# Performance work log

Measured on AMD Instinct MI355X. Metric: run time of the kernel, lower is better.

The kernel has to match this reference:

```python
import jax, jax.numpy as jnp
import numpy as np

N, E, B = 100000, 3200000, 512
D_IN, D_H, HID = 500, 64, 200
NUM_CLASSES = 80
EPS_BN = 1e-5


def _sage(x, src, dst, Wl, bl, Wr):
    # PyG SAGEConv (mean aggr): out = lin_l(mean_{j->i} x_j) + lin_r(x_i)
    n = x.shape[0]
    agg = jax.ops.segment_sum(x[src], dst, num_segments=n)          # [n, d_in]
    deg = jax.ops.segment_sum(jnp.ones((src.shape[0],), x.dtype), dst, num_segments=n)
    mean = agg / jnp.maximum(deg, 1.0)[:, None]
    return mean @ Wl + bl + x @ Wr


def _bn(c, g, b):
    # BatchNorm1d, training-mode batch statistics (biased var)
    mu = c.mean(0)
    var = c.var(0)
    return (c - mu) / jnp.sqrt(var + EPS_BN) * g + b


def setup_inputs() -> dict:
    key = jax.random.key(0)
    ks = jax.random.split(key, 16)
    p = lambda k, shape: jax.random.normal(k, shape, dtype=jnp.float32) * 0.05
    z = lambda d: jnp.zeros((d,), jnp.float32)
    o = lambda d: jnp.ones((d,), jnp.float32)
    return {
        "x": jax.random.uniform(ks[0], (N, D_IN), dtype=jnp.float32),
        "edge_index": jax.random.randint(ks[1], (2, E), 0, N),
        "batch": jnp.sort(jax.random.randint(ks[2], (N,), 0, B)),
        "y": jax.random.randint(ks[3], (B,), 0, NUM_CLASSES),
        "conv1_Wl": p(ks[4], (D_IN, D_H)), "conv1_bl": z(D_H), "conv1_Wr": p(ks[5], (D_IN, D_H)),
        "conv2_Wl": p(ks[6], (D_H, D_H)),  "conv2_bl": z(D_H), "conv2_Wr": p(ks[7], (D_H, D_H)),
        "conv3_Wl": p(ks[8], (D_H, D_H)),  "conv3_bl": z(D_H), "conv3_Wr": p(ks[9], (D_H, D_H)),
        "lin1_W": p(ks[10], (D_H, HID)), "lin1_b": z(HID),
        "bn1_g": o(HID), "bn1_beta": z(HID),
        "lin2_W": p(ks[11], (HID, HID // 2)), "lin2_b": z(HID // 2),
        "bn2_g": o(HID // 2), "bn2_beta": z(HID // 2),
        "lin3_W": p(ks[12], (HID // 2, HID // 2)), "lin3_b": z(HID // 2),
        "bn3_g": o(HID // 2), "bn3_beta": z(HID // 2),
        "lin4_W": p(ks[13], (HID // 2, NUM_CLASSES)), "lin4_b": z(NUM_CLASSES),
    }


def reference(x, edge_index, batch, y,
              conv1_Wl, conv1_bl, conv1_Wr,
              conv2_Wl, conv2_bl, conv2_Wr,
              conv3_Wl, conv3_bl, conv3_Wr,
              lin1_W, lin1_b, bn1_g, bn1_beta,
              lin2_W, lin2_b, bn2_g, bn2_beta,
              lin3_W, lin3_b, bn3_g, bn3_beta,
              lin4_W, lin4_b):
    src, dst = edge_index[0], edge_index[1]
    # F.normalize(x, p=1.0, dim=-1)
    xn = x / jnp.maximum(jnp.abs(x).sum(-1, keepdims=True), 1e-12)
    e = _sage(xn, src, dst, conv1_Wl, conv1_bl, conv1_Wr)
    e = _sage(e, src, dst, conv2_Wl, conv2_bl, conv2_Wr)
    e = _sage(e, src, dst, conv3_Wl, conv3_bl, conv3_Wr)
    # global_mean_pool over graph ids
    sums = jax.ops.segment_sum(e, batch, num_segments=B)             # [B, 64]
    cnts = jax.ops.segment_sum(jnp.ones((e.shape[0],), e.dtype), batch, num_segments=B)
    c = sums / jnp.maximum(cnts, 1.0)[:, None]
    # dropout (p=0.1) omitted for a deterministic reference
    c = c @ lin1_W + lin1_b
    b = jnp.tanh(_bn(c, bn1_g, bn1_beta))
    c = b @ lin2_W + lin2_b
    b = jnp.tanh(_bn(c, bn2_g, bn2_beta))
    c = b @ lin3_W + lin3_b
    b = jnp.tanh(_bn(c, bn3_g, bn3_beta))
    return b @ lin4_W + lin4_b                                       # [B, 80]
```

## Files before the change

### kernel.cpp

```cpp
#include <hip/hip_runtime.h>
#include <hip/hip_bf16.h>

#define NN 100000
#define NE 3200000
#define NB 512
#define DIN 500
#define DH 64
#define HIDN 200
#define NCLS 80

#define NBUK 256
#define NPB 391
#define EPB 16384
#define NBLK_E ((NE + EPB - 1) / EPB)

typedef __attribute__((ext_vector_type(8))) short bf16x8;
typedef __attribute__((ext_vector_type(4))) float f32x4;

__device__ __forceinline__ short f2bf(float f) {
    union { float f; unsigned u; } v; v.f = f;
    unsigned r = v.u + 0x7FFF + ((v.u >> 16) & 1);
    return (short)(r >> 16);
}
__device__ __forceinline__ float bf2f(short s) {
    union { unsigned u; float f; } v; v.u = ((unsigned)(unsigned short)s) << 16;
    return v.f;
}

__global__ void bukhist_kernel(const int* __restrict__ dst, int* __restrict__ block_hist) {
    __shared__ int h[NBUK];
    for (int i = threadIdx.x; i < NBUK; i += 256) h[i] = 0;
    __syncthreads();
    int base = blockIdx.x * EPB;
    int end = min(base + EPB, NE);
    for (int e = base + threadIdx.x; e < end; e += 256)
        atomicAdd(&h[dst[e] / NPB], 1);
    __syncthreads();
    for (int i = threadIdx.x; i < NBUK; i += 256)
        block_hist[blockIdx.x * NBUK + i] = h[i];
}

__global__ void bukoff_kernel(int* __restrict__ block_hist, int* __restrict__ buk_base) {
    __shared__ int tot[NBUK];
    __shared__ int sc[NBUK];
    int b = threadIdx.x;
    int s = 0;
    for (int i = 0; i < NBLK_E; ++i) s += block_hist[i * NBUK + b];
    tot[b] = s; sc[b] = s;
    __syncthreads();
    for (int o = 1; o < NBUK; o <<= 1) {
        int t = (b >= o) ? sc[b - o] : 0;
        __syncthreads();
        sc[b] += t;
        __syncthreads();
    }
    int excl = sc[b] - tot[b];
    buk_base[b] = excl;
    if (b == NBUK - 1) buk_base[NBUK] = excl + tot[b];
    int run = excl;
    for (int i = 0; i < NBLK_E; ++i) {
        int idx = i * NBUK + b;
        int v = block_hist[idx];
        block_hist[idx] = run;
        run += v;
    }
}

__global__ void bukscat_kernel(const int* __restrict__ src, const int* __restrict__ dst,
                               const int* __restrict__ block_hist, int* __restrict__ bpack) {
    __shared__ int cur[NBUK];
    for (int i = threadIdx.x; i < NBUK; i += 256)
        cur[i] = block_hist[blockIdx.x * NBUK + i];
    __syncthreads();
    int base = blockIdx.x * EPB;
    int end = min(base + EPB, NE);
    for (int e = base + threadIdx.x; e < end; e += 256) {
        int d = dst[e];
        int bk = d / NPB;
        int p = atomicAdd(&cur[bk], 1);
        bpack[p] = (src[e] << 9) | (d - bk * NPB);
    }
}

__global__ void bukfin_kernel(const int* __restrict__ buk_base, const int* __restrict__ bpack,
                              int* __restrict__ row_ptr, float* __restrict__ invdeg,
                              int* __restrict__ csr_src) {
    __shared__ int cnt[NPB];
    __shared__ int cbase[NPB];
    int bk = blockIdx.x;
    int n0 = bk * NPB;
    int nloc = min(n0 + NPB, NN) - n0;
    for (int i = threadIdx.x; i < nloc; i += 256) cnt[i] = 0;
    __syncthreads();
    int beg = buk_base[bk], end = buk_base[bk + 1];
    for (int p = beg + threadIdx.x; p < end; p += 256)
        atomicAdd(&cnt[bpack[p] & 511], 1);
    __syncthreads();
    if (threadIdx.x == 0) {
        int run = beg;
        for (int i = 0; i < nloc; ++i) { int v = cnt[i]; cbase[i] = run; run += v; }
    }
    __syncthreads();
    for (int i = threadIdx.x; i < nloc; i += 256) {
        row_ptr[n0 + i] = cbase[i];
        invdeg[n0 + i] = 1.0f / fmaxf((float)cnt[i], 1.0f);
        cnt[i] = cbase[i];
    }
    if (bk == NBUK - 1 && threadIdx.x == 0) row_ptr[NN] = end;
    __syncthreads();
    for (int p = beg + threadIdx.x; p < end; p += 256) {
        int v = bpack[p];
        int q = atomicAdd(&cnt[v & 511], 1);
        csr_src[q] = v >> 9;
    }
}

__global__ void wprep_kernel(const float* __restrict__ Wl, const float* __restrict__ Wr,
                             short* __restrict__ Wb, int K, int KP) {
    int id = blockIdx.x * blockDim.x + threadIdx.x;
    if (id >= 128 * KP) return;
    int col = id / KP, k = id - col * KP;
    float v = 0.f;
    if (k < K) v = (col < 64) ? Wl[(size_t)k * 64 + col] : Wr[(size_t)k * 64 + (col - 64)];
    Wb[(size_t)col * KP + k] = f2bf(v);
}

__launch_bounds__(256)
__global__ void gemm_mfma_pipe(const float* __restrict__ in, const short* __restrict__ Wb,
                               short* __restrict__ Hl, float* __restrict__ Hr) {
    __shared__ short A_lds[2][128][40];
    __shared__ short B_lds[2][128][40];
    __shared__ float s_red[128][2];
    const int tid = threadIdx.x;
    const int row0 = blockIdx.x * 128;
    const int w = tid >> 6, l = tid & 63;
    const int q = l >> 4, r16 = l & 15;
    const int sa_row = tid >> 1;
    const int sa_kc  = (tid & 1) * 16;
    const int ga_row = row0 + sa_row;
    const bool row_ok = ga_row < NN;
    const float* arow = in + (size_t)ga_row * DIN + sa_kc;
    const short* bsrc = Wb + (size_t)sa_row * 512 + sa_kc;

    f32x4 acc0[8], acc1[8];
#pragma unroll
    for (int c = 0; c < 8; ++c) { acc0[c] = (f32x4){0.f,0.f,0.f,0.f}; acc1[c] = (f32x4){0.f,0.f,0.f,0.f}; }
    float pabs = 0.f;
    float va0[16], va1[16];
    bf16x8 vb00, vb01, vb10, vb11;

#define ISSUE(T, S) do { \
    _Pragma("unroll") \
    for (int i = 0; i < 16; i += 4) { \
        int gk = (T) * 32 + sa_kc + i; \
        float4 f = (row_ok && gk < DIN) ? *(const float4*)(arow + (T) * 32 + i) \
                                        : make_float4(0.f, 0.f, 0.f, 0.f); \
        va##S[i] = f.x; va##S[i+1] = f.y; va##S[i+2] = f.z; va##S[i+3] = f.w; \
    } \
    vb##S##0 = *(const bf16x8*)(bsrc + (T) * 32); \
    vb##S##1 = *(const bf16x8*)(bsrc + (T) * 32 + 8); \
} while (0)

#define STAGE(BUF, S) do { \
    short sh[16]; \
    _Pragma("unroll") \
    for (int i = 0; i < 16; ++i) { pabs += fabsf(va##S[i]); sh[i] = f2bf(va##S[i]); } \
    *(bf16x8*)&A_lds[BUF][sa_row][sa_kc]     = *(bf16x8*)&sh[0]; \
    *(bf16x8*)&A_lds[BUF][sa_row][sa_kc + 8] = *(bf16x8*)&sh[8]; \
    *(bf16x8*)&B_lds[BUF][sa_row][sa_kc]     = vb##S##0; \
    *(bf16x8*)&B_lds[BUF][sa_row][sa_kc + 8] = vb##S##1; \
} while (0)

#define COMPUTE(BUF) do { \
    bf16x8 a0 = *(bf16x8*)&A_lds[BUF][w * 32 + r16][q * 8]; \
    bf16x8 a1 = *(bf16x8*)&A_lds[BUF][w * 32 + 16 + r16][q * 8]; \
    _Pragma("unroll") \
    for (int c = 0; c < 8; ++c) { \
        bf16x8 b = *(bf16x8*)&B_lds[BUF][c * 16 + r16][q * 8]; \
        acc0[c] = __builtin_amdgcn_mfma_f32_16x16x32_bf16(a0, b, acc0[c], 0, 0, 0); \
        acc1[c] = __builtin_amdgcn_mfma_f32_16x16x32_bf16(a1, b, acc1[c], 0, 0, 0); \
    } \
} while (0)

    ISSUE(0, 0); ISSUE(1, 1);
    STAGE(0, 0);
    __syncthreads();
    for (int tt = 0; tt < 8; ++tt) {
        int t0 = tt * 2;
        if (tt < 7) ISSUE(t0 + 2, 0);
        COMPUTE(0);
        STAGE(1, 1);
        __syncthreads();
        if (tt < 7) ISSUE(t0 + 3, 1);
        COMPUTE(1);
        if (tt < 7) { STAGE(0, 0); __syncthreads(); }
    }
#undef ISSUE
#undef STAGE
#undef COMPUTE

    __syncthreads();
    s_red[sa_row][tid & 1] = pabs;
    __syncthreads();
    if (tid < 128) {
        float ss = s_red[tid][0] + s_red[tid][1];
        s_red[tid][0] = 1.0f / fmaxf(ss, 1e-12f);
    }
    __syncthreads();

#define EPI(RF, ACC) do { \
    _Pragma("unroll") \
    for (int c = 0; c < 8; ++c) { \
        _Pragma("unroll") \
        for (int rr = 0; rr < 4; ++rr) { \
            int lrow = w * 32 + (RF) * 16 + q * 4 + rr; \
            int grow = row0 + lrow; \
            if (grow < NN) { \
                float o = ACC[c][rr] * s_red[lrow][0]; \
                if (c < 4) Hl[(size_t)grow * 64 + c * 16 + r16] = f2bf(o); \
                else       Hr[(size_t)grow * 64 + (c - 4) * 16 + r16] = o; \
            } \
        } \
    } \
} while (0)
    EPI(0, acc0);
    EPI(1, acc1);
#undef EPI
}

__launch_bounds__(256)
__global__ void gemm64_mfma(const short* __restrict__ ein, const short* __restrict__ Wb,
                            short* __restrict__ Hl, float* __restrict__ Hr) {
    const int tid = threadIdx.x;
    const int row0 = blockIdx.x * 64;
    const int w = tid >> 6, l = tid & 63;
    const int q = l >> 4, r16 = l & 15;
    const int arow = row0 + w * 16 + r16;
    const bool ok = arow < NN;
    const short* ap = ein + (size_t)(ok ? arow : 0) * 64 + q * 8;
    f32x4 acc[8];
#pragma unroll
    for (int c = 0; c < 8; ++c) acc[c] = (f32x4){0.f, 0.f, 0.f, 0.f};
    const bf16x8 z8 = (bf16x8){0, 0, 0, 0, 0, 0, 0, 0};
#pragma unroll
    for (int t = 0; t < 2; ++t) {
        bf16x8 a = ok ? *(const bf16x8*)(ap + t * 32) : z8;
#pragma unroll
        for (int c = 0; c < 8; ++c) {
            bf16x8 b = *(const bf16x8*)(Wb + (size_t)(c * 16 + r16) * 64 + t * 32 + q * 8);
            acc[c] = __builtin_amdgcn_mfma_f32_16x16x32_bf16(a, b, acc[c], 0, 0, 0);
        }
    }
#pragma unroll
    for (int c = 0; c < 8; ++c) {
#pragma unroll
        for (int rr = 0; rr < 4; ++rr) {
            int grow = row0 + w * 16 + q * 4 + rr;
            if (grow < NN) {
                if (c < 4) Hl[(size_t)grow * 64 + c * 16 + r16] = f2bf(acc[c][rr]);
                else       Hr[(size_t)grow * 64 + (c - 4) * 16 + r16] = acc[c][rr];
            }
        }
    }
}

template<bool LAST>
__launch_bounds__(256, 8)
__global__ void gather_kernel(const int* __restrict__ row_ptr, const int* __restrict__ csr_src,
                              const short* __restrict__ Hl, const float* __restrict__ Hr,
                              const float* __restrict__ invdeg, const float* __restrict__ bl,
                              short* __restrict__ ebf, float* __restrict__ ef32) {
    int node = blockIdx.x * 4 + (threadIdx.x >> 6);
    if (node >= NN) return;
    int lane = threadIdx.x & 63;
    int ng = lane >> 3;
    int fl = lane & 7;
    int beg = row_ptr[node], end = row_ptr[node + 1];
    float a0[8], a1[8];
#pragma unroll
    for (int j = 0; j < 8; ++j) { a0[j] = 0.f; a1[j] = 0.f; }
    int p = beg + ng;
    for (; p + 24 < end; p += 32) {
        int s0 = csr_src[p];
        int s1 = csr_src[p + 8];
        int s2 = csr_src[p + 16];
        int s3 = csr_src[p + 24];
        bf16x8 v0 = *(const bf16x8*)(Hl + (size_t)s0 * 64 + fl * 8);
        bf16x8 v1 = *(const bf16x8*)(Hl + (size_t)s1 * 64 + fl * 8);
        bf16x8 v2 = *(const bf16x8*)(Hl + (size_t)s2 * 64 + fl * 8);
        bf16x8 v3 = *(const bf16x8*)(Hl + (size_t)s3 * 64 + fl * 8);
#pragma unroll
        for (int j = 0; j < 8; ++j) {
            a0[j] += bf2f(v0[j]) + bf2f(v2[j]);
            a1[j] += bf2f(v1[j]) + bf2f(v3[j]);
        }
    }
    for (; p < end; p += 8) {
        int s0 = csr_src[p];
        bf16x8 v0 = *(const bf16x8*)(Hl + (size_t)s0 * 64 + fl * 8);
#pragma unroll
        for (int j = 0; j < 8; ++j) a0[j] += bf2f(v0[j]);
    }
#pragma unroll
    for (int j = 0; j < 8; ++j) a0[j] += a1[j];
#pragma unroll
    for (int m = 8; m < 64; m <<= 1)
#pragma unroll
        for (int j = 0; j < 8; ++j) a0[j] += __shfl_xor(a0[j], m, 64);
    if (ng == 0) {
        float idg = invdeg[node];
        const float4 h0 = *(const float4*)(Hr + (size_t)node * 64 + fl * 8);
        const float4 h1 = *(const float4*)(Hr + (size_t)node * 64 + fl * 8 + 4);
        float o[8];
        o[0] = a0[0] * idg + bl[fl * 8 + 0] + h0.x;
        o[1] = a0[1] * idg + bl[fl * 8 + 1] + h0.y;
        o[2] = a0[2] * idg + bl[fl * 8 + 2] + h0.z;
        o[3] = a0[3] * idg + bl[fl * 8 + 3] + h0.w;
        o[4] = a0[4] * idg + bl[fl * 8 + 4] + h1.x;
        o[5] = a0[5] * idg + bl[fl * 8 + 5] + h1.y;
        o[6] = a0[6] * idg + bl[fl * 8 + 6] + h1.z;
        o[7] = a0[7] * idg + bl[fl * 8 + 7] + h1.w;
        if (LAST) {
            *(float4*)(ef32 + (size_t)node * 64 + fl * 8)     = make_float4(o[0], o[1], o[2], o[3]);
            *(float4*)(ef32 + (size_t)node * 64 + fl * 8 + 4) = make_float4(o[4], o[5], o[6], o[7]);
        } else {
            short s[8];
#pragma unroll
            for (int j = 0; j < 8; ++j) s[j] = f2bf(o[j]);
            *(bf16x8*)(ebf + (size_t)node * 64 + fl * 8) = *(bf16x8*)s;
        }
    }
}

__global__ void gseg_kernel(const int* __restrict__ batch, int* __restrict__ gstart) {
    int i = blockIdx.x * blockDim.x + threadIdx.x;
    if (i >= NN) return;
    int bc = batch[i];
    int bp = (i == 0) ? -1 : batch[i - 1];
    for (int b = bp + 1; b <= bc; ++b) gstart[b] = i;
    if (i == NN - 1)
        for (int b = bc + 1; b <= NB; ++b) gstart[b] = NN;
}

__launch_bounds__(256)
__global__ void pool_seg(const float* __restrict__ e, const int* __restrict__ gstart,
                         float* __restrict__ c0) {
    __shared__ float part[4][64];
    int b = blockIdx.x;
    int w = threadIdx.x >> 6, lane = threadIdx.x & 63;
    int s = gstart[b], t = gstart[b + 1];
    float acc = 0.f;
    for (int i = s + w; i < t; i += 4) acc += e[(size_t)i * 64 + lane];
    part[w][lane] = acc;
    __syncthreads();
    if (w == 0) {
        float v = part[0][lane] + part[1][lane] + part[2][lane] + part[3][lane];
        c0[b * 64 + lane] = v / fmaxf((float)(t - s), 1.0f);
    }
}

__global__ void lin_kernel(const float* __restrict__ in, const float* __restrict__ W,
                           const float* __restrict__ bias, float* __restrict__ out,
                           int Kd, int Dout) {
    int id = blockIdx.x * blockDim.x + threadIdx.x;
    if (id >= NB * Dout) return;
    int row = id / Dout, col = id - row * Dout;
    const float* ir = in + (size_t)row * Kd;
    float acc = bias[col];
    for (int k = 0; k < Kd; ++k) acc += ir[k] * W[(size_t)k * Dout + col];
    out[id] = acc;
}

__global__ void bnstats_kernel(const float* __restrict__ c, const float* __restrict__ g,
                               const float* __restrict__ beta, float* __restrict__ sa,
                               float* __restrict__ sb, int Dout) {
    int col = blockIdx.x;
    int tid = threadIdx.x;
    float s = 0.f, sq = 0.f;
    for (int r = tid; r < NB; r += 256) {
        float v = c[(size_t)r * Dout + col];
        s += v; sq += v * v;
    }
    __shared__ float ls[256], lq[256];
    ls[tid] = s; lq[tid] = sq;
    __syncthreads();
    for (int o = 128; o > 0; o >>= 1) {
        if (tid < o) { ls[tid] += ls[tid + o]; lq[tid] += lq[tid + o]; }
        __syncthreads();
    }
    if (tid == 0) {
        float mu = ls[0] / NB;
        float var = lq[0] / NB - mu * mu;
        float a = g[col] * rsqrtf(var + 1e-5f);
        sa[col] = a;
        sb[col] = beta[col] - mu * a;
    }
}

__global__ void bnapply_kernel(const float* __restrict__ c, const float* __restrict__ sa,
                               const float* __restrict__ sb, float* __restrict__ bv, int Dout) {
    int id = blockIdx.x * blockDim.x + threadIdx.x;
    if (id >= NB * Dout) return;
    int col = id % Dout;
    bv[id] = tanhf(c[id] * sa[col] + sb[col]);
}

extern "C" void kernel_launch(void* const* d_in, const int* in_sizes, int n_in,
                              void* d_out, int out_size, void* d_ws, size_t ws_size,
                              hipStream_t stream) {
    const float* x    = (const float*)d_in[0];
    const int* ei     = (const int*)d_in[1];
    const int* src    = ei;
    const int* dst    = ei + NE;
    const int* batch  = (const int*)d_in[2];
    const float* c1Wl = (const float*)d_in[4];
    const float* c1bl = (const float*)d_in[5];
    const float* c1Wr = (const float*)d_in[6];
    const float* c2Wl = (const float*)d_in[7];
    const float* c2bl = (const float*)d_in[8];
    const float* c2Wr = (const float*)d_in[9];
    const float* c3Wl = (const float*)d_in[10];
    const float* c3bl = (const float*)d_in[11];
    const float* c3Wr = (const float*)d_in[12];
    const float* l1W  = (const float*)d_in[13]; const float* l1b = (const float*)d_in[14];
    const float* bn1g = (const float*)d_in[15]; const float* bn1b = (const float*)d_in[16];
    const float* l2W  = (const float*)d_in[17]; const float* l2b = (const float*)d_in[18];
    const float* bn2g = (const float*)d_in[19]; const float* bn2b = (const float*)d_in[20];
    const float* l3W  = (const float*)d_in[21]; const float* l3b = (const float*)d_in[22];
    const float* bn3g = (const float*)d_in[23]; const float* bn3b = (const float*)d_in[24];
    const float* l4W  = (const float*)d_in[25]; const float* l4b = (const float*)d_in[26];
    float* out = (float*)d_out;

    char* wsb = (char*)d_ws;
    short* Hl     = (short*)wsb; wsb += (size_t)NN * 64 * 2;
    float* Hr     = (float*)wsb; wsb += (size_t)NN * 64 * 4;
    short* e      = (short*)wsb; wsb += (size_t)NN * 64 * 2;
    float* e3     = (float*)wsb; wsb += (size_t)NN * 64 * 4;
    float* invdeg = (float*)wsb; wsb += (size_t)NN * 4;
    float* c      = (float*)wsb; wsb += (size_t)NB * HIDN * 4;
    float* bv     = (float*)wsb; wsb += (size_t)NB * HIDN * 4;
    float* sa     = (float*)wsb; wsb += HIDN * 4;
    float* sb     = (float*)wsb; wsb += HIDN * 4;
    short* Wb1    = (short*)wsb; wsb += 128 * 512 * 2;
    short* Wb2    = (short*)wsb; wsb += 128 * 64 * 2;
    short* Wb3    = (short*)wsb; wsb += 128 * 64 * 2;
    int* row_ptr  = (int*)wsb;   wsb += (size_t)(NN + 1) * 4;
    int* csr_src  = (int*)wsb;   wsb += (size_t)NE * 4;
    int* buk_base = (int*)wsb;   wsb += (NBUK + 1) * 4;
    int* gstart   = (int*)wsb;   wsb += (NB + 1) * 4;
    int* bpack      = (int*)Hl;
    int* block_hist = (int*)e;

    bukhist_kernel<<<NBLK_E, 256, 0, stream>>>(dst, block_hist);
    bukoff_kernel<<<1, NBUK, 0, stream>>>(block_hist, buk_base);
    bukscat_kernel<<<NBLK_E, 256, 0, stream>>>(src, dst, block_hist, bpack);
    bukfin_kernel<<<NBUK, 256, 0, stream>>>(buk_base, bpack, row_ptr, invdeg, csr_src);

    gseg_kernel<<<(NN + 255) / 256, 256, 0, stream>>>(batch, gstart);

    wprep_kernel<<<(128 * 512 + 255) / 256, 256, 0, stream>>>(c1Wl, c1Wr, Wb1, DIN, 512);
    wprep_kernel<<<(128 * 64 + 255) / 256, 256, 0, stream>>>(c2Wl, c2Wr, Wb2, DH, 64);
    wprep_kernel<<<(128 * 64 + 255) / 256, 256, 0, stream>>>(c3Wl, c3Wr, Wb3, DH, 64);

    const int GB128 = (NN + 127) / 128;
    const int GB64  = (NN + 63) / 64;
    const int GGB   = (NN + 3) / 4;

    gemm_mfma_pipe<<<GB128, 256, 0, stream>>>(x, Wb1, Hl, Hr);
    gather_kernel<false><<<GGB, 256, 0, stream>>>(row_ptr, csr_src, Hl, Hr, invdeg, c1bl, e, e3);
    gemm64_mfma<<<GB64, 256, 0, stream>>>(e, Wb2, Hl, Hr);
    gather_kernel<false><<<GGB, 256, 0, stream>>>(row_ptr, csr_src, Hl, Hr, invdeg, c2bl, e, e3);
    gemm64_mfma<<<GB64, 256, 0, stream>>>(e, Wb3, Hl, Hr);
    gather_kernel<true><<<GGB, 256, 0, stream>>>(row_ptr, csr_src, Hl, Hr, invdeg, c3bl, e, e3);

    pool_seg<<<NB, 256, 0, stream>>>(e3, gstart, bv);

    lin_kernel<<<(NB * 200 + 255) / 256, 256, 0, stream>>>(bv, l1W, l1b, c, 64, 200);
    bnstats_kernel<<<200, 256, 0, stream>>>(c, bn1g, bn1b, sa, sb, 200);
    bnapply_kernel<<<(NB * 200 + 255) / 256, 256, 0, stream>>>(c, sa, sb, bv, 200);

    lin_kernel<<<(NB * 100 + 255) / 256, 256, 0, stream>>>(bv, l2W, l2b, c, 200, 100);
    bnstats_kernel<<<100, 256, 0, stream>>>(c, bn2g, bn2b, sa, sb, 100);
    bnapply_kernel<<<(NB * 100 + 255) / 256, 256, 0, stream>>>(c, sa, sb, bv, 100);

    lin_kernel<<<(NB * 100 + 255) / 256, 256, 0, stream>>>(bv, l3W, l3b, c, 100, 100);
    bnstats_kernel<<<100, 256, 0, stream>>>(c, bn3g, bn3b, sa, sb, 100);
    bnapply_kernel<<<(NB * 100 + 255) / 256, 256, 0, stream>>>(c, sa, sb, bv, 100);

    lin_kernel<<<(NB * 80 + 255) / 256, 256, 0, stream>>>(bv, l4W, l4b, out, 100, 80);
}
```

Before: 608.4 us.

## Replace LDS double-buffered first-layer GEMM with direct register-fed MFMA

The first SAGE layer GEMM no longer stages x and the bf16 weights through double-buffered shared memory. Each lane now loads its MFMA A fragment straight from global memory and reads weight fragments directly from global, which L1/L2 should serve. The row L1-norm is reduced with wave shuffles instead of a shared-memory reduction. Blocks shrink to 64 rows, which removes all barriers and LDS use but adds repeated weight reads from cache and less coalesced x loads.

```diff
diff --git a/kernel.cpp b/kernel.cpp
--- a/kernel.cpp
+++ b/kernel.cpp
@@ -126,106 +126,65 @@
 }
 
 __launch_bounds__(256)
-__global__ void gemm_mfma_pipe(const float* __restrict__ in, const short* __restrict__ Wb,
-                               short* __restrict__ Hl, float* __restrict__ Hr) {
-    __shared__ short A_lds[2][128][40];
-    __shared__ short B_lds[2][128][40];
-    __shared__ float s_red[128][2];
+__global__ void gemm_direct(const float* __restrict__ in, const short* __restrict__ Wb,
+                            short* __restrict__ Hl, float* __restrict__ Hr) {
     const int tid = threadIdx.x;
-    const int row0 = blockIdx.x * 128;
     const int w = tid >> 6, l = tid & 63;
     const int q = l >> 4, r16 = l & 15;
-    const int sa_row = tid >> 1;
-    const int sa_kc  = (tid & 1) * 16;
-    const int ga_row = row0 + sa_row;
-    const bool row_ok = ga_row < NN;
-    const float* arow = in + (size_t)ga_row * DIN + sa_kc;
-    const short* bsrc = Wb + (size_t)sa_row * 512 + sa_kc;
-
-    f32x4 acc0[8], acc1[8];
-#pragma unroll
-    for (int c = 0; c < 8; ++c) { acc0[c] = (f32x4){0.f,0.f,0.f,0.f}; acc1[c] = (f32x4){0.f,0.f,0.f,0.f}; }
+    const int tile0 = blockIdx.x * 64 + w * 16;
+    const int arow_i = tile0 + r16;
+    const bool ok = arow_i < NN;
+    const float* arow = in + (size_t)(ok ? arow_i : 0) * DIN + q * 8;
+
+    f32x4 acc[8];
+#pragma unroll
+    for (int c = 0; c < 8; ++c) acc[c] = (f32x4){0.f, 0.f, 0.f, 0.f};
     float pabs = 0.f;
-    float va0[16], va1[16];
-    bf16x8 vb00, vb01, vb10, vb11;
-
-#define ISSUE(T, S) do { \
-    _Pragma("unroll") \
-    for (int i = 0; i < 16; i += 4) { \
-        int gk = (T) * 32 + sa_kc + i; \
-        float4 f = (row_ok && gk < DIN) ? *(const float4*)(arow + (T) * 32 + i) \
-                                        : make_float4(0.f, 0.f, 0.f, 0.f); \
-        va##S[i] = f.x; va##S[i+1] = f.y; va##S[i+2] = f.z; va##S[i+3] = f.w; \
-    } \
-    vb##S##0 = *(const bf16x8*)(bsrc + (T) * 32); \
-    vb##S##1 = *(const bf16x8*)(bsrc + (T) * 32 + 8); \
-} while (0)
-
-#define STAGE(BUF, S) do { \
-    short sh[16]; \
-    _Pragma("unroll") \
-    for (int i = 0; i < 16; ++i) { pabs += fabsf(va##S[i]); sh[i] = f2bf(va##S[i]); } \
-    *(bf16x8*)&A_lds[BUF][sa_row][sa_kc]     = *(bf16x8*)&sh[0]; \
-    *(bf16x8*)&A_lds[BUF][sa_row][sa_kc + 8] = *(bf16x8*)&sh[8]; \
-    *(bf16x8*)&B_lds[BUF][sa_row][sa_kc]     = vb##S##0; \
-    *(bf16x8*)&B_lds[BUF][sa_row][sa_kc + 8] = vb##S##1; \
-} while (0)
-
-#define COMPUTE(BUF) do { \
-    bf16x8 a0 = *(bf16x8*)&A_lds[BUF][w * 32 + r16][q * 8]; \
-    bf16x8 a1 = *(bf16x8*)&A_lds[BUF][w * 32 + 16 + r16][q * 8]; \
-    _Pragma("unroll") \
-    for (int c = 0; c < 8; ++c) { \
-        bf16x8 b = *(bf16x8*)&B_lds[BUF][c * 16 + r16][q * 8]; \
-        acc0[c] = __builtin_amdgcn_mfma_f32_16x16x32_bf16(a0, b, acc0[c], 0, 0, 0); \
-        acc1[c] = __builtin_amdgcn_mfma_f32_16x16x32_bf16(a1, b, acc1[c], 0, 0, 0); \
-    } \
-} while (0)
-
-    ISSUE(0, 0); ISSUE(1, 1);
-    STAGE(0, 0);
-    __syncthreads();
-    for (int tt = 0; tt < 8; ++tt) {
-        int t0 = tt * 2;
-        if (tt < 7) ISSUE(t0 + 2, 0);
-        COMPUTE(0);
-        STAGE(1, 1);
-        __syncthreads();
-        if (tt < 7) ISSUE(t0 + 3, 1);
-        COMPUTE(1);
-        if (tt < 7) { STAGE(0, 0); __syncthreads(); }
-    }
-#undef ISSUE
-#undef STAGE
-#undef COMPUTE
-
-    __syncthreads();
-    s_red[sa_row][tid & 1] = pabs;
-    __syncthreads();
-    if (tid < 128) {
-        float ss = s_red[tid][0] + s_red[tid][1];
-        s_red[tid][0] = 1.0f / fmaxf(ss, 1e-12f);
-    }
-    __syncthreads();
-
-#define EPI(RF, ACC) do { \
-    _Pragma("unroll") \
-    for (int c = 0; c < 8; ++c) { \
-        _Pragma("unroll") \
-        for (int rr = 0; rr < 4; ++rr) { \
-            int lrow = w * 32 + (RF) * 16 + q * 4 + rr; \
-            int grow = row0 + lrow; \
-            if (grow < NN) { \
-                float o = ACC[c][rr] * s_red[lrow][0]; \
-                if (c < 4) Hl[(size_t)grow * 64 + c * 16 + r16] = f2bf(o); \
-                else       Hr[(size_t)grow * 64 + (c - 4) * 16 + r16] = o; \
-            } \
-        } \
-    } \
-} while (0)
-    EPI(0, acc0);
-    EPI(1, acc1);
-#undef EPI
+
+#pragma unroll
+    for (int t = 0; t < 16; ++t) {
+        float v[8];
+        if (t < 15) {
+            const float4 f0 = *(const float4*)(arow + t * 32);
+            const float4 f1 = *(const float4*)(arow + t * 32 + 4);
+            v[0] = f0.x; v[1] = f0.y; v[2] = f0.z; v[3] = f0.w;
+            v[4] = f1.x; v[5] = f1.y; v[6] = f1.z; v[7] = f1.w;
+        } else {
+#pragma unroll
+            for (int i = 0; i < 8; ++i) {
+                int gk = t * 32 + q * 8 + i;
+                v[i] = (gk < DIN) ? arow[t * 32 + i] : 0.f;
+            }
+        }
+        short sh[8];
+#pragma unroll
+        for (int i = 0; i < 8; ++i) { pabs += fabsf(v[i]); sh[i] = f2bf(v[i]); }
+        bf16x8 a = *(bf16x8*)sh;
+#pragma unroll
+        for (int c = 0; c < 8; ++c) {
+            bf16x8 b = *(const bf16x8*)(Wb + (size_t)(c * 16 + r16) * 512 + t * 32 + q * 8);
+            acc[c] = __builtin_amdgcn_mfma_f32_16x16x32_bf16(a, b, acc[c], 0, 0, 0);
+        }
+    }
+
+    pabs += __shfl_xor(pabs, 16, 64);
+    pabs += __shfl_xor(pabs, 32, 64);
+    float sval = 1.0f / fmaxf(pabs, 1e-12f);
+
+#pragma unroll
+    for (int rr = 0; rr < 4; ++rr) {
+        int lrow = q * 4 + rr;
+        float srow = __shfl(sval, lrow, 64);
+        int grow = tile0 + lrow;
+        if (grow < NN) {
+#pragma unroll
+            for (int c = 0; c < 8; ++c) {
+                float o = acc[c][rr] * srow;
+                if (c < 4) Hl[(size_t)grow * 64 + c * 16 + r16] = f2bf(o);
+                else       Hr[(size_t)grow * 64 + (c - 4) * 16 + r16] = o;
+            }
+        }
+    }
 }
 
 __launch_bounds__(256)
@@ -462,11 +421,10 @@
     wprep_kernel<<<(128 * 64 + 255) / 256, 256, 0, stream>>>(c2Wl, c2Wr, Wb2, DH, 64);
     wprep_kernel<<<(128 * 64 + 255) / 256, 256, 0, stream>>>(c3Wl, c3Wr, Wb3, DH, 64);
 
-    const int GB128 = (NN + 127) / 128;
-    const int GB64  = (NN + 63) / 64;
-    const int GGB   = (NN + 3) / 4;
-
-    gemm_mfma_pipe<<<GB128, 256, 0, stream>>>(x, Wb1, Hl, Hr);
+    const int GB64 = (NN + 63) / 64;
+    const int GGB  = (NN + 3) / 4;
+
+    gemm_direct<<<GB64, 256, 0, stream>>>(x, Wb1, Hl, Hr);
     gather_kernel<false><<<GGB, 256, 0, stream>>>(row_ptr, csr_src, Hl, Hr, invdeg, c1bl, e, e3);
     gemm64_mfma<<<GB64, 256, 0, stream>>>(e, Wb2, Hl, Hr);
     gather_kernel<false><<<GGB, 256, 0, stream>>>(row_ptr, csr_src, Hl, Hr, invdeg, c2bl, e, e3);
```

New measurement: 652.0 us. +7.2%, slower.
